# Performance work log

Measured on AMD Instinct MI355X. Metric: run time of the kernel, lower is better.

## Reference

```python
import jax, jax.numpy as jnp
import numpy as np

B, N, M, U, L = 2048, 256, 128, 512, 2   # batch, memory locations, memory width, num_units, num_layers
RH, WH, SH = 2, 2, 1                      # read heads, write heads, conv_shift_range
CLIP = 20.0
HEAD_R = M + 3 + (2 * SH + 1)             # 134 = k(M)+beta+g+s(2r+1)+gamma
HEAD_W = HEAD_R + 2 * M                   # 390 = + erase(M) + add(M)


def setup_inputs():
    key = jax.random.key(0)
    ks = jax.random.split(key, 12)
    def nrm(k, shape, s=0.05):
        return jax.random.normal(k, shape, jnp.float32) * s
    return {
        "X": jax.random.normal(ks[0], (B, U), jnp.float32),
        "m0": nrm(ks[1], (1, N, M), 0.5),
        "H0": nrm(ks[2], (L, 1, U)),
        "C0": nrm(ks[3], (L, 1, U)),
        "R0": nrm(ks[4], (RH, 1, M)),
        "A0": nrm(ks[5], (RH + WH, 1, N)),
        "W_prep": nrm(ks[6], (M * RH, U)),
        "b_prep": jnp.zeros((U,), jnp.float32),
        "W_lstm": nrm(ks[7], (L, 3 * U, 4 * U)),
        "b_lstm": jnp.zeros((L, 4 * U), jnp.float32),
        "W_r": nrm(ks[8], (U, RH * HEAD_R)),
        "b_r": jnp.zeros((RH * HEAD_R,), jnp.float32),
        "W_w": nrm(ks[9], (U, WH * HEAD_W)),
        "b_w": jnp.zeros((WH * HEAD_W,), jnp.float32),
        "W_ou": nrm(ks[10], (U + RH * M, U)),
        "b_ou": jnp.zeros((U,), jnp.float32),
    }


def _addressing(k, beta, g, s, gamma, m, a_prev):
    # k [B,M], beta/g/gamma [B], s [B,2*SH+1], m [B,N,M], a_prev [B,N]
    inner = jnp.einsum('bnm,bm->bn', m, k)
    k_norm = jnp.sqrt(jnp.sum(k * k, axis=1, keepdims=True))   # [B,1]
    m_norm = jnp.sqrt(jnp.sum(m * m, axis=2))                  # [B,N]
    K = inner / (k_norm * m_norm + 1e-8)
    w_c = jax.nn.softmax(beta[:, None] * K, axis=1)            # exp/sum in source == softmax
    w_g = g[:, None] * w_c + (1.0 - g[:, None]) * a_prev
    # The stacked-slice s_matrix in the source is exactly circular convolution:
    # w_conv[i] = sum_d s_d * w_g[(i - d) mod N], d in {0..SH, -SH..-1} matching s layout.
    shifts = list(range(0, SH + 1)) + list(range(-SH, 0))
    w_conv = sum(s[:, j:j + 1] * jnp.roll(w_g, shifts[j], axis=1) for j in range(2 * SH + 1))
    w_sharp = w_conv ** gamma[:, None]
    return w_sharp / jnp.sum(w_sharp, axis=1, keepdims=True)


def reference(X, m0, H0, C0, R0, A0, W_prep, b_prep, W_lstm, b_lstm,
              W_r, b_r, W_w, b_w, W_ou, b_ou):
    b = X.shape[0]
    m = jnp.broadcast_to(m0, (b, N, M))
    R_prev = [jnp.broadcast_to(jnp.tanh(R0[i]), (b, M)) for i in range(RH)]
    A_prev = [jnp.broadcast_to(jax.nn.softmax(A0[i], axis=-1), (b, N)) for i in range(RH + WH)]

    # controller
    h = jnp.concatenate(R_prev, axis=1) @ W_prep + b_prep
    for l in range(L):
        x_in = jnp.concatenate([X, h], axis=1)                              # [B,2U]
        h_prev = jnp.broadcast_to(H0[l], (b, U))
        c_prev = jnp.broadcast_to(C0[l], (b, U))
        z = jnp.concatenate([x_in, h_prev], axis=1) @ W_lstm[l] + b_lstm[l]  # [B,4U]
        i_g, f_g, g_g, o_g = jnp.split(z, 4, axis=1)
        c = jax.nn.sigmoid(f_g) * c_prev + jax.nn.sigmoid(i_g) * jnp.tanh(g_g)
        h = jax.nn.sigmoid(o_g) * jnp.tanh(c)
    h = jnp.clip(h, -CLIP, CLIP)

    r_heads = (h @ W_r + b_r).reshape(b, RH, HEAD_R)
    w_heads = (h @ W_w + b_w).reshape(b, WH, HEAD_W)
    heads = [r_heads[:, i] for i in range(RH)] + [w_heads[:, i] for i in range(WH)]

    A_t = []
    for ii, hd in enumerate(heads):
        A_t.append(_addressing(
            k=jnp.tanh(hd[:, :M]),
            beta=jax.nn.softplus(hd[:, M]),
            g=jax.nn.sigmoid(hd[:, M + 1]),
            s=jax.nn.softmax(hd[:, M + 2:M + 2 + 2 * SH + 1], axis=-1),
            gamma=jax.nn.softplus(hd[:, M + 2 + 2 * SH + 1]),
            m=m, a_prev=A_prev[ii]))

    # reads from old memory
    R_t = [jnp.einsum('bn,bnm->bm', A_t[i], m) for i in range(RH)]

    # sequential erase/add writes
    m_t = m
    for ii in range(WH):
        w = A_t[RH + ii][:, :, None]                                  # [B,N,1]
        del_v = jax.nn.sigmoid(w_heads[:, ii, -2 * M:-M])[:, None, :]  # [B,1,M]
        add_v = jnp.tanh(w_heads[:, ii, -M:])[:, None, :]
        m_t = m_t * (1.0 - w * del_v) + w * add_v

    y = jnp.clip(jnp.concatenate([h] + R_t, axis=1) @ W_ou + b_ou, -CLIP, CLIP)
    return y, m_t
```

## Files before the change

kernel.cpp:

```cpp
#include <hip/hip_runtime.h>
#include <math.h>

static constexpr int Bn = 2048;
static constexpr int Nn = 256;
static constexpr int Mn = 128;
static constexpr int Un = 512;

static constexpr size_t OFF_MNORM = 4608;
static constexpr size_t OFF_APREV = 4864;
static constexpr size_t OFF_BIASH = 5888;
static constexpr size_t OFF_KMAT  = 16384;
static constexpr size_t OFF_HEADS = OFF_KMAT + 2097152;
static constexpr size_t OFF_AT    = OFF_HEADS + 2146304;
static constexpr size_t OFF_ERA   = OFF_AT + 1048576;
static constexpr size_t OFF_ADD   = OFF_ERA + 524288;
static constexpr size_t OFF_XHB   = OFF_ADD + 524288;
static constexpr size_t OFF_HCAT  = OFF_XHB + 1048576;
static constexpr size_t OFF_W0T   = OFF_HCAT + 1048576;
static constexpr size_t OFF_W1T   = OFF_W0T + 524288;
static constexpr size_t OFF_WRWT  = OFF_W1T + 1048576;
static constexpr size_t OFF_WCOMB = OFF_WRWT + 294912;
static constexpr size_t OFF_WR2T  = OFF_WCOMB + 262144;
static constexpr size_t OFF_M0B   = OFF_WR2T + 65536;
static constexpr size_t OFF_ZPART = OFF_M0B + 16384;
static constexpr size_t OFF_YH    = OFF_ZPART + 32768;

static constexpr int P_X0  = 0;
static constexpr int P_M0  = 512;
static constexpr int P_W0  = 528;
static constexpr int P_W1  = 1552;
static constexpr int P_WR2 = 3600;
static constexpr int P_CA  = 3728;
static constexpr int P_ZC  = 3729;
static constexpr int P_END = 3793;

static constexpr int M_L0  = 0;
static constexpr int M_ZX  = 512;
static constexpr int M_PF  = 1024;
static constexpr int M_WRr = 1056;
static constexpr int M_WRw = 1200;
static constexpr int M_WOU = 1600;
static constexpr int M_ZC1 = 1856;
static constexpr int M_END = 1920;

static constexpr int H_HD  = 0;
static constexpr int H_YH  = 288;
static constexpr int H_END = 416;

static constexpr int T_OUT = 0;
static constexpr int T_MEM = 128;
static constexpr int T_END = 384;

#define DEV __device__ __forceinline__

typedef __attribute__((ext_vector_type(8))) short bf16x8;
typedef __attribute__((ext_vector_type(4))) float f32x4;
typedef __attribute__((ext_vector_type(8))) unsigned short ushort8;
typedef unsigned int u32;

DEV float sigf(float x) { return 1.0f / (1.0f + expf(-x)); }
DEV float softplusf(float x) { return x > 20.0f ? x : log1pf(expf(x)); }
DEV unsigned short f2bf(float f) {
    unsigned u = __float_as_uint(f);
    u = (u + 0x7FFFu + ((u >> 16) & 1u)) >> 16;
    return (unsigned short)u;
}
DEV float b2f(unsigned short u) { return __uint_as_float((u32)u << 16); }
DEV void gload16(const unsigned short* g, unsigned short* l) {
    __builtin_amdgcn_global_load_lds(
        (const __attribute__((address_space(1))) u32*)g,
        (__attribute__((address_space(3))) u32*)l, 16, 0, 0);
}

DEV float blk_reduce_max(float v, float* red) {
    int tid = threadIdx.x;
    red[tid] = v; __syncthreads();
    for (int s = (int)blockDim.x >> 1; s > 0; s >>= 1) {
        if (tid < s) red[tid] = fmaxf(red[tid], red[tid + s]);
        __syncthreads();
    }
    float r = red[0]; __syncthreads();
    return r;
}
DEV float blk_reduce_sum(float v, float* red) {
    int tid = threadIdx.x;
    red[tid] = v; __syncthreads();
    for (int s = (int)blockDim.x >> 1; s > 0; s >>= 1) {
        if (tid < s) red[tid] += red[tid + s];
        __syncthreads();
    }
    float r = red[0]; __syncthreads();
    return r;
}

DEV float wv_sum(float v) {
    #pragma unroll
    for (int off = 32; off; off >>= 1) v += __shfl_xor(v, off);
    return v;
}
DEV float wv_max(float v) {
    #pragma unroll
    for (int off = 32; off; off >>= 1) v = fmaxf(v, __shfl_xor(v, off));
    return v;
}
DEV float blk_sum4(float v, float* red4) {
    v = wv_sum(v);
    int w = threadIdx.x >> 6;
    if ((threadIdx.x & 63) == 0) red4[w] = v;
    __syncthreads();
    float r = red4[0] + red4[1] + red4[2] + red4[3];
    __syncthreads();
    return r;
}
DEV float blk_max4(float v, float* red4) {
    v = wv_max(v);
    int w = threadIdx.x >> 6;
    if ((threadIdx.x & 63) == 0) red4[w] = v;
    __syncthreads();
    float r = fmaxf(fmaxf(red4[0], red4[1]), fmaxf(red4[2], red4[3]));
    __syncthreads();
    return r;
}

#define GEMM_SHARED                                                             \
    __shared__ __align__(16) unsigned short As[2][64 * 64];                     \
    __shared__ __align__(16) unsigned short Ws[2][128 * 64];

#define GEMM_REGS                                                               \
    const int tid  = threadIdx.x;                                               \
    const int lane = tid & 63;                                                  \
    const int wave = tid >> 6;                                                  \
    const int wr = wave >> 1, wc = wave & 1;                                    \
    const int ke = ((tid & 7) * 8) ^ (((tid >> 3) & 7) << 3);                   \
    const int frow = lane & 15;                                                 \
    const int fko  = (lane >> 4) * 8;                                           \
    const int fxm  = (frow & 7) << 3;                                           \
    f32x4 acc[2][4];                                                            \
    _Pragma("unroll")                                                           \
    for (int i = 0; i < 2; ++i)                                                 \
        _Pragma("unroll")                                                       \
        for (int j = 0; j < 4; ++j) acc[i][j] = (f32x4){0.f, 0.f, 0.f, 0.f};

#define GEMM_STAGE(buf, k0)                                                     \
    {                                                                           \
        _Pragma("unroll")                                                       \
        for (int q = 0; q < 2; ++q)                                             \
            gload16(A  + (size_t)(row0 + q * 32 + (tid >> 3)) * lda + (k0) + ke,\
                    &As[buf][q * 2048 + tid * 8]);                              \
        _Pragma("unroll")                                                       \
        for (int q = 0; q < 4; ++q)                                             \
            gload16(Wt + (size_t)(col0 + q * 32 + (tid >> 3)) * ldw + (k0) + ke,\
                    &Ws[buf][q * 2048 + tid * 8]);                              \
    }

#define GEMM_FRAGS_AND_MFMA(Ab, Wb)                                             \
    {                                                                           \
        bf16x8 af[2][2], wf[2][4];                                              \
        _Pragma("unroll")                                                       \
        for (int kk = 0; kk < 2; ++kk) {                                        \
            _Pragma("unroll")                                                   \
            for (int i = 0; i < 2; ++i) {                                       \
                int fr = wr * 32 + i * 16 + frow;                               \
                af[kk][i] = *(const bf16x8*)&(Ab)[fr * 64 + ((kk * 32 + fko) ^ fxm)]; \
            }                                                                   \
            _Pragma("unroll")                                                   \
            for (int j = 0; j < 4; ++j) {                                       \
                int fr = wc * 64 + j * 16 + frow;                               \
                wf[kk][j] = *(const bf16x8*)&(Wb)[fr * 64 + ((kk * 32 + fko) ^ fxm)]; \
            }                                                                   \
        }                                                                       \
        __builtin_amdgcn_s_setprio(1);                                          \
        _Pragma("unroll")                                                       \
        for (int kk = 0; kk < 2; ++kk)                                          \
            _Pragma("unroll")                                                   \
            for (int i = 0; i < 2; ++i)                                         \
                _Pragma("unroll")                                               \
                for (int j = 0; j < 4; ++j)                                     \
                    acc[i][j] = __builtin_amdgcn_mfma_f32_16x16x32_bf16(        \
                        af[kk][i], wf[kk][j], acc[i][j], 0, 0, 0);              \
        __builtin_amdgcn_s_setprio(0);                                          \
    }

#define GEMM_MAINLOOP(Kr)                                                       \
    {                                                                           \
        const int nt = (Kr) >> 6;                                               \
        int cur = 0;                                                            \
        GEMM_STAGE(0, 0);                                                       \
        for (int t = 0; t < nt; ++t) {                                          \
            if (t + 1 < nt) {                                                   \
                GEMM_STAGE(cur ^ 1, (t + 1) * 64);                              \
                asm volatile("s_waitcnt vmcnt(6)" ::: "memory");                \
            } else {                                                            \
                asm volatile("s_waitcnt vmcnt(0)" ::: "memory");                \
            }                                                                   \
            __builtin_amdgcn_sched_barrier(0);                                  \
            __builtin_amdgcn_s_barrier();                                       \
            __builtin_amdgcn_sched_barrier(0);                                  \
            GEMM_FRAGS_AND_MFMA(As[cur], Ws[cur]);                              \
            __builtin_amdgcn_sched_barrier(0);                                  \
            __builtin_amdgcn_s_barrier();                                       \
            cur ^= 1;                                                           \
        }                                                                       \
    }

#define LSTM_EPILOGUE(zc, doclip, houtp, ldhv, ZXP)                             \
    {                                                                           \
        const int uu = lane & 15;                                               \
        const int q  = (col0 >> 6) + wc;                                        \
        const int uq = q * 16 + uu;                                             \
        const float c0v = c0[(zc) * 512 + uq];                                  \
        float bg[4];                                                            \
        _Pragma("unroll")                                                       \
        for (int g = 0; g < 4; ++g) {                                           \
            int j = g * 512 + q * 16 + uu;                                      \
            float a = b_lstm[(zc) * 2048 + j];                                  \
            _Pragma("unroll")                                                   \
            for (int p = 0; p < 8; ++p)                                         \
                a += zpart[((size_t)(zc) * 8 + p) * 2048 + j];                  \
            bg[g] = a;                                                          \
        }                                                                       \
        _Pragma("unroll")                                                       \
        for (int i = 0; i < 2; ++i) {                                           \
            int rbase = row0 + wr * 32 + i * 16 + (lane >> 4) * 4;              \
            _Pragma("unroll")                                                   \
            for (int r = 0; r < 4; ++r) {                                       \
                float z0 = 0.f, z1 = 0.f, z2 = 0.f, z3 = 0.f;                   \
                if (ZXP) {                                                      \
                    const unsigned short* zr = (ZXP) +                          \
                        (size_t)(rbase + r) * 2048 + q * 64 + uu;               \
                    z0 = b2f(zr[0]);  z1 = b2f(zr[16]);                         \
                    z2 = b2f(zr[32]); z3 = b2f(zr[48]);                         \
                }                                                               \
                float ig = acc[i][0][r] + bg[0] + z0;                           \
                float fg = acc[i][1][r] + bg[1] + z1;                           \
                float gg = acc[i][2][r] + bg[2] + z2;                           \
                float og = acc[i][3][r] + bg[3] + z3;                           \
                float c = sigf(fg) * c0v + sigf(ig) * tanhf(gg);                \
                float h = sigf(og) * tanhf(c);                                  \
                if (doclip) h = fminf(fmaxf(h, -20.f), 20.f);                   \
                (houtp)[(size_t)(rbase + r) * (ldhv) + uq] = f2bf(h);           \
            }                                                                   \
        }                                                                       \
    }

DEV void dev_cvt8(const float* src, int lds, unsigned short* dst, int ldd,
                  int c8, int bloc, int tid)
{
    size_t idx = (size_t)bloc * 256 + tid;
    size_t r = idx / c8, c = (idx % c8) * 8;
    const float* s = src + r * lds + c;
    float4 v0 = *(const float4*)s;
    float4 v1 = *(const float4*)(s + 4);
    ushort8 o;
    o[0] = f2bf(v0.x); o[1] = f2bf(v0.y); o[2] = f2bf(v0.z); o[3] = f2bf(v0.w);
    o[4] = f2bf(v1.x); o[5] = f2bf(v1.y); o[6] = f2bf(v1.z); o[7] = f2bf(v1.w);
    *(ushort8*)(dst + r * ldd + c) = o;
}

DEV void dev_cvtT(const float* src, int R, int C, int lds,
                  unsigned short* dst, int ldd, int mode, int bx, int by,
                  int tid, float* t )
{
    const int x = tid & 31;
    for (int y = tid >> 5; y < 32; y += 8) {
        int r = by * 32 + y, c = bx * 32 + x;
        int scol = c;
        if (mode) scol = ((c >> 4) & 3) * 512 + (c >> 6) * 16 + (c & 15);
        t[y * 33 + x] = (r < R && c < C) ? src[(size_t)r * lds + scol] : 0.f;
    }
    __syncthreads();
    for (int y = tid >> 5; y < 32; y += 8) {
        int c = bx * 32 + y, r = by * 32 + x;
        if (c < C && r < R) dst[(size_t)c * ldd + r] = f2bf(t[x * 33 + y]);
    }
}

__global__ __launch_bounds__(256) void k_prep(
    const float* __restrict__ X, const float* __restrict__ m0,
    const float* __restrict__ H0, const float* __restrict__ R0,
    const float* __restrict__ A0, const float* __restrict__ W_prep,
    const float* __restrict__ b_prep, const float* __restrict__ W_lstm,
    const float* __restrict__ b_r, const float* __restrict__ b_w,
    const float* __restrict__ W_ou, float* __restrict__ ws)
{
    __shared__ float sh[32 * 33 + 64];
    const int bid = blockIdx.x, tid = threadIdx.x;
    unsigned short* XHB  = (unsigned short*)(ws + OFF_XHB);
    unsigned short* W0T  = (unsigned short*)(ws + OFF_W0T);
    unsigned short* W1T  = (unsigned short*)(ws + OFF_W1T);
    unsigned short* WR2T = (unsigned short*)(ws + OFF_WR2T);
    unsigned short* M0B  = (unsigned short*)(ws + OFF_M0B);

    if (bid < P_M0) {
        dev_cvt8(X, 512, XHB, 1024, 64, bid - P_X0, tid);
    } else if (bid < P_W0) {
        dev_cvt8(m0, 128, M0B, 128, 16, bid - P_M0, tid);
    } else if (bid < P_W1) {
        int s = bid - P_W0;
        dev_cvtT(W_lstm, 512, 2048, 2048, W0T, 512, 1, s & 63, s >> 6, tid, sh);
    } else if (bid < P_WR2) {
        int s = bid - P_W1;
        dev_cvtT(W_lstm + (size_t)1536 * 2048, 1024, 2048, 2048, W1T, 1024, 1,
                 s & 63, s >> 6, tid, sh);
    } else if (bid < P_CA) {
        int s = bid - P_WR2;
        dev_cvtT(W_ou + (size_t)512 * 512, 256, 512, 512, WR2T, 256, 0,
                 s & 15, s >> 4, tid, sh);
    } else if (bid < P_ZC) {
        float* red = sh;
        for (int i = 0; i < 4; ++i) {
            float v = A0[i * 256 + tid];
            float mx = blk_reduce_max(v, red);
            float e = expf(v - mx);
            float s = blk_reduce_sum(e, red);
            ws[OFF_APREV + i * 256 + tid] = e / s;
        }
        float acc = 0.f;
        for (int m = 0; m < 128; ++m) {
            float t = m0[(size_t)tid * 128 + m];
            acc = fmaf(t, t, acc);
        }
        ws[OFF_MNORM + tid] = sqrtf(acc);
        for (int j = tid; j < 1152; j += 256)
            ws[OFF_BIASH + j] = (j < 268) ? b_r[j] : (j < 1048 ? b_w[j - 268] : 0.f);
    } else {
        int sub = bid - P_ZC;
        int colb = sub & 7, up = sub >> 3;
        int j = colb * 256 + tid;
        float acc = 0.f;
        if (up < 4) {
            sh[256 + tid] = tanhf(R0[tid]);
            __syncthreads();
            if (tid < 128) {
                int u = up * 128 + tid;
                float a = b_prep[u];
                for (int k = 0; k < 256; ++k)
                    a = fmaf(sh[256 + k], W_prep[(size_t)k * 512 + u], a);
                sh[tid] = a;
            }
            __syncthreads();
            const int u0 = up * 128;
            #pragma unroll 4
            for (int t = 0; t < 128; ++t)
                acc = fmaf(sh[t], W_lstm[(size_t)(512 + u0 + t) * 2048 + j], acc);
        } else {
            const int u0 = up * 128;
            #pragma unroll 4
            for (int t = 0; t < 128; ++t)
                acc = fmaf(H0[u0 - 512 + t],
                           W_lstm[(size_t)(512 + u0 + t) * 2048 + j], acc);
        }
        (ws + OFF_ZPART)[(size_t)up * 2048 + j] = acc;
    }
}

__global__ __launch_bounds__(256) void k_mid(
    const float* __restrict__ W_lstm, const float* __restrict__ W_r,
    const float* __restrict__ W_w, const float* __restrict__ W_ou,
    const float* __restrict__ H0, const float* __restrict__ b_lstm,
    const float* __restrict__ c0, float* __restrict__ ws)
{
    GEMM_SHARED
    const int s = blockIdx.x;
    float* sh = (float*)&As[0][0];
    unsigned short* XHB   = (unsigned short*)(ws + OFF_XHB);
    unsigned short* W0T   = (unsigned short*)(ws + OFF_W0T);
    unsigned short* W1T   = (unsigned short*)(ws + OFF_W1T);
    unsigned short* WRWT  = (unsigned short*)(ws + OFF_WRWT);
    unsigned short* WCOMB = (unsigned short*)(ws + OFF_WCOMB);
    unsigned short* WR2T  = (unsigned short*)(ws + OFF_WR2T);
    unsigned short* M0B   = (unsigned short*)(ws + OFF_M0B);
    unsigned short* ZX    = (unsigned short*)(ws + OFF_KMAT);
    const float* zpart    = ws + OFF_ZPART;

    if (s < M_WRr) {
        const unsigned short *A, *Wt;
        int lda, ldw, row0, col0, Kr, mode;
        unsigned short* pCb = nullptr;
        if (s < M_ZX) {
            mode = 0;
            A = XHB;  lda = 1024; Wt = W0T; ldw = 512;
            row0 = (s & 31) * 64; col0 = (s >> 5) * 128; Kr = 512;
        } else if (s < M_PF) {
            int p = s - M_ZX;
            mode = 1;
            A = XHB;  lda = 1024; Wt = W1T; ldw = 1024;
            row0 = (p & 31) * 64; col0 = (p >> 5) * 128; Kr = 512;
        } else {
            int p = s - M_PF;
            mode = 2;
            int pz = p >> 4, py = (p >> 3) & 1, px = p & 7;
            A = WR2T + pz * 128; lda = 256; Wt = M0B; ldw = 128;
            row0 = px * 64; col0 = py * 128; Kr = 128;
            pCb = WCOMB + 512 + pz * 256;
        }
        GEMM_REGS
        GEMM_MAINLOOP(Kr)
        if (mode == 0) {
            unsigned short* hout = XHB + 512;
            const unsigned short* zxn = nullptr;
            LSTM_EPILOGUE(0, 0, hout, 1024, zxn)
        } else if (mode == 1) {
            #pragma unroll
            for (int i = 0; i < 2; ++i) {
                int m0r = row0 + wr * 32 + i * 16 + (lane >> 4) * 4;
                #pragma unroll
                for (int j = 0; j < 4; ++j) {
                    int n = col0 + wc * 64 + j * 16 + (lane & 15);
                    #pragma unroll
                    for (int r = 0; r < 4; ++r)
                        ZX[(size_t)(m0r + r) * 2048 + n] = f2bf(acc[i][j][r]);
                }
            }
        } else {
            #pragma unroll
            for (int i = 0; i < 2; ++i) {
                int m0r = row0 + wr * 32 + i * 16 + (lane >> 4) * 4;
                #pragma unroll
                for (int j = 0; j < 4; ++j) {
                    int n = col0 + wc * 64 + j * 16 + (lane & 15);
                    #pragma unroll
                    for (int r = 0; r < 4; ++r)
                        pCb[(size_t)(m0r + r) * 1024 + n] = f2bf(acc[i][j][r]);
                }
            }
        }
    } else if (s < M_WRw) {
        int s2 = s - M_WRr;
        dev_cvtT(W_r, 512, 268, 268, WRWT, 512, 0, s2 % 9, s2 / 9, threadIdx.x, sh);
    } else if (s < M_WOU) {
        int s3 = s - M_WRw;
        dev_cvtT(W_w, 512, 780, 780, WRWT + (size_t)268 * 512, 512, 0,
                 s3 % 25, s3 / 25, threadIdx.x, sh);
    } else if (s < M_ZC1) {
        int s4 = s - M_WOU;
        dev_cvtT(W_ou, 512, 512, 512, WCOMB, 1024, 0, s4 & 15, s4 >> 4,
                 threadIdx.x, sh);
    } else {
        int s5 = s - M_ZC1;
        int colb = s5 & 7, up = s5 >> 3;
        int j = colb * 256 + threadIdx.x;
        const int u0 = up * 64;
        const float* W1 = W_lstm + (size_t)1536 * 2048;
        float acc = 0.f;
        #pragma unroll 4
        for (int t = 0; t < 64; ++t)
            acc = fmaf(H0[512 + u0 + t], W1[(size_t)(1024 + u0 + t) * 2048 + j], acc);
        (ws + OFF_ZPART)[((size_t)8 + up) * 2048 + j] = acc;
    }
}

__global__ __launch_bounds__(256) void gemm_lstm(
    const unsigned short* __restrict__ A, int lda,
    const unsigned short* __restrict__ Wt, int ldw,
    const float* __restrict__ zpart, const float* __restrict__ b_lstm,
    const float* __restrict__ c0, const unsigned short* __restrict__ ZXP,
    unsigned short* __restrict__ hout)
{
    GEMM_SHARED
    const int row0 = blockIdx.x * 64;
    const int col0 = blockIdx.y * 128;
    GEMM_REGS
    GEMM_MAINLOOP(512)
    LSTM_EPILOGUE(1, 1, hout, 1024, ZXP)
}

__global__ __launch_bounds__(256) void k_heads(
    const unsigned short* __restrict__ HCAT,
    const unsigned short* __restrict__ WRWT,
    const unsigned short* __restrict__ WCOMB,
    const float* __restrict__ biash,
    float* __restrict__ heads, float* __restrict__ yh)
{
    GEMM_SHARED
    const int s = blockIdx.x;
    const unsigned short* A = HCAT;  const int lda = 1024;
    const unsigned short* Wt;
    int ldw, row0, col0;
    if (s < H_YH) {
        Wt = WRWT; ldw = 512;
        row0 = (s & 31) * 64; col0 = (s >> 5) * 128;
    } else {
        int p = s - H_YH;
        Wt = WCOMB; ldw = 1024;
        row0 = (p & 31) * 64; col0 = (p >> 5) * 128;
    }
    GEMM_REGS
    GEMM_MAINLOOP(512)
    if (s < H_YH) {
        #pragma unroll
        for (int i = 0; i < 2; ++i) {
            int m0r = row0 + wr * 32 + i * 16 + (lane >> 4) * 4;
            #pragma unroll
            for (int j = 0; j < 4; ++j) {
                int n = col0 + wc * 64 + j * 16 + (lane & 15);
                if (n >= 1048) continue;
                float bv = biash[n];
                #pragma unroll
                for (int r = 0; r < 4; ++r)
                    heads[(size_t)(m0r + r) * 1048 + n] = acc[i][j][r] + bv;
            }
        }
    } else {
        #pragma unroll
        for (int i = 0; i < 2; ++i) {
            int m0r = row0 + wr * 32 + i * 16 + (lane >> 4) * 4;
            #pragma unroll
            for (int j = 0; j < 4; ++j) {
                int n = col0 + wc * 64 + j * 16 + (lane & 15);
                #pragma unroll
                for (int r = 0; r < 4; ++r)
                    yh[(size_t)(m0r + r) * 512 + n] = acc[i][j][r];
            }
        }
    }
}

__global__ __launch_bounds__(256) void gemm_kmat(
    const float* __restrict__ heads,
    const unsigned short* __restrict__ M0B,
    float* __restrict__ C)
{
    GEMM_SHARED
    const int row0 = blockIdx.x * 64;
    const int col0 = blockIdx.y * 128;
    GEMM_REGS

#define KMAT_STAGE(buf, k0)                                                     \
    {                                                                           \
        _Pragma("unroll")                                                       \
        for (int q = 0; q < 2; ++q) {                                           \
            int R = row0 + q * 32 + (tid >> 3);                                 \
            int b = R >> 2, ih = R & 3;                                         \
            int cb = (ih < 2) ? ih * 134 : 268 + (ih - 2) * 390;                \
            const float* hp = heads + (size_t)b * 1048 + cb + (k0) + ke;        \
            ushort8 o;                                                          \
            _Pragma("unroll")                                                   \
            for (int j = 0; j < 8; ++j) o[j] = f2bf(tanhf(hp[j]));              \
            *(ushort8*)&As[buf][q * 2048 + tid * 8] = o;                        \
        }                                                                       \
        _Pragma("unroll")                                                       \
        for (int q = 0; q < 4; ++q)                                             \
            gload16(M0B + (size_t)(col0 + q * 32 + (tid >> 3)) * 128 + (k0) + ke,\
                    &Ws[buf][q * 2048 + tid * 8]);                              \
    }

    int cur = 0;
    KMAT_STAGE(0, 0);
    for (int t = 0; t < 2; ++t) {
        __syncthreads();
        if (t == 0) KMAT_STAGE(1, 64);
        GEMM_FRAGS_AND_MFMA(As[cur], Ws[cur]);
        cur ^= 1;
    }
#undef KMAT_STAGE
    #pragma unroll
    for (int i = 0; i < 2; ++i) {
        int m0r = row0 + wr * 32 + i * 16 + (lane >> 4) * 4;
        #pragma unroll
        for (int j = 0; j < 4; ++j) {
            int n = col0 + wc * 64 + j * 16 + (lane & 15);
            #pragma unroll
            for (int r = 0; r < 4; ++r)
                C[(size_t)(m0r + r) * 256 + n] = acc[i][j][r];
        }
    }
}

__global__ __launch_bounds__(256) void k_addr(
    const float* __restrict__ heads, const float* __restrict__ kmat,
    const float* __restrict__ mnorm, const float* __restrict__ aprev,
    float* __restrict__ at, unsigned short* __restrict__ hcat,
    float* __restrict__ era, float* __restrict__ addv)
{
    __shared__ float red4[4];
    __shared__ float wgs[256];
    __shared__ float sc[6];
    const int b = blockIdx.x, i = blockIdx.y, tid = threadIdx.x;
    const int cb = (i < 2) ? i * 134 : 268 + (i - 2) * 390;
    const float* hd = heads + (size_t)b * 1048 + cb;
    float kv = (tid < 128) ? tanhf(hd[tid]) : 0.f;
    float kn = sqrtf(blk_sum4(kv * kv, red4));
    if (i >= 2 && tid < 128) {
        era [((size_t)b * 2 + (i - 2)) * 128 + tid] = sigf(hd[134 + tid]);
        addv[((size_t)b * 2 + (i - 2)) * 128 + tid] = tanhf(hd[262 + tid]);
    }
    if (tid == 0) {
        sc[0] = softplusf(hd[128]);
        sc[1] = sigf(hd[129]);
        float v0 = hd[130], v1 = hd[131], v2 = hd[132];
        float mx = fmaxf(v0, fmaxf(v1, v2));
        float e0 = expf(v0 - mx), e1 = expf(v1 - mx), e2 = expf(v2 - mx);
        float ssum = e0 + e1 + e2;
        sc[2] = e0 / ssum; sc[3] = e1 / ssum; sc[4] = e2 / ssum;
        sc[5] = softplusf(hd[133]);
    }
    __syncthreads();
    const float beta = sc[0], g = sc[1], s0 = sc[2], s1 = sc[3], s2 = sc[4],
                gamma = sc[5];
    float inner = kmat[((size_t)b * 4 + i) * 256 + tid];
    float K = inner / (kn * mnorm[tid] + 1e-8f);
    float x = beta * K;
    float mx = blk_max4(x, red4);
    float e = expf(x - mx);
    float se = blk_sum4(e, red4);
    float wc = e / se;
    float wg = g * wc + (1.f - g) * aprev[i * 256 + tid];
    wgs[tid] = wg;
    __syncthreads();
    float wconv = s0 * wg + s1 * wgs[(tid + 255) & 255] + s2 * wgs[(tid + 1) & 255];
    float wsh = powf(wconv, gamma);
    float ssum = blk_sum4(wsh, red4);
    float w = wsh / ssum;
    if (i < 2) hcat[(size_t)b * 1024 + 512 + i * 256 + tid] = f2bf(w);
    else       at[((size_t)(i - 2) * Bn + b) * 256 + tid] = w;
}

__global__ __launch_bounds__(256) void k_tail(
    const unsigned short* __restrict__ HCAT,
    const unsigned short* __restrict__ WCOMB,
    const float* __restrict__ yh, const float* __restrict__ b_ou,
    const float* __restrict__ m0, const float* __restrict__ at,
    const float* __restrict__ era, const float* __restrict__ addv,
    float* __restrict__ out)
{
    GEMM_SHARED
    const int s = blockIdx.x;
    if (s < T_MEM) {
        const unsigned short* A  = HCAT + 512;        const int lda = 1024;
        const unsigned short* Wt = WCOMB + 512;       const int ldw = 1024;
        const int row0 = (s & 31) * 64;
        const int col0 = (s >> 5) * 128;
        GEMM_REGS
        GEMM_MAINLOOP(512)
        #pragma unroll
        for (int i = 0; i < 2; ++i) {
            int m0r = row0 + wr * 32 + i * 16 + (lane >> 4) * 4;
            #pragma unroll
            for (int j = 0; j < 4; ++j) {
                int n = col0 + wc * 64 + j * 16 + (lane & 15);
                if (n >= 512) continue;
                float bv = b_ou[n];
                #pragma unroll
                for (int r = 0; r < 4; ++r) {
                    float v = acc[i][j][r] + bv + yh[(size_t)(m0r + r) * 512 + n];
                    out[(size_t)(m0r + r) * 512 + n] = fminf(fmaxf(v, -20.f), 20.f);
                }
            }
        }
    } else {
        const int tid = threadIdx.x;
        const int b0 = (s - T_MEM) * 8;
        float (*at_s)[8][256] = (float(*)[8][256])(&As[0][0]);
        float (*er_s)[8][128] = (float(*)[8][128])(&Ws[0][0]);
        float (*ad_s)[8][128] = (float(*)[8][128])(&Ws[0][4096]);
        for (int t = tid; t < 1024; t += 256) {
            int i = t >> 9, rem = t & 511;
            int bb = rem >> 6, n4 = rem & 63;
            ((float4*)&at_s[i][bb][0])[n4] =
                ((const float4*)(at + ((size_t)i * Bn + b0 + bb) * 256))[n4];
        }
        for (int t = tid; t < 512; t += 256) {
            int i = t >> 8, rem = t & 255;
            int bb = rem >> 5, m4 = rem & 31;
            ((float4*)&er_s[i][bb][0])[m4] =
                ((const float4*)(era + ((size_t)(b0 + bb) * 2 + i) * 128))[m4];
            ((float4*)&ad_s[i][bb][0])[m4] =
                ((const float4*)(addv + ((size_t)(b0 + bb) * 2 + i) * 128))[m4];
        }
        __syncthreads();
        const float4* m0v = (const float4*)m0;
        float4* outv = (float4*)(out + (size_t)Bn * Un);
        for (int pos = tid; pos < 8192; pos += 256) {
            int mq = pos & 31, n = pos >> 5;
            float4 t0 = m0v[pos];
            #pragma unroll
            for (int bb = 0; bb < 8; ++bb) {
                float w0 = at_s[0][bb][n], w1 = at_s[1][bb][n];
                float4 e0 = *(const float4*)&er_s[0][bb][mq * 4];
                float4 a0 = *(const float4*)&ad_s[0][bb][mq * 4];
                float4 e1 = *(const float4*)&er_s[1][bb][mq * 4];
                float4 a1 = *(const float4*)&ad_s[1][bb][mq * 4];
                float4 t = t0;
#define UPD(c) { t.c = t.c * (1.f - w0 * e0.c) + w0 * a0.c; \
                 t.c = t.c * (1.f - w1 * e1.c) + w1 * a1.c; }
                UPD(x) UPD(y) UPD(z) UPD(w)
#undef UPD
                __builtin_nontemporal_store(*(f32x4*)&t,
                    (f32x4*)&outv[(size_t)(b0 + bb) * 8192 + pos]);
            }
        }
    }
}

extern "C" void kernel_launch(void* const* d_in, const int* in_sizes, int n_in,
                              void* d_out, int out_size, void* d_ws, size_t ws_size,
                              hipStream_t stream)
{
    const float* X      = (const float*)d_in[0];
    const float* m0     = (const float*)d_in[1];
    const float* H0     = (const float*)d_in[2];
    const float* C0     = (const float*)d_in[3];
    const float* R0     = (const float*)d_in[4];
    const float* A0     = (const float*)d_in[5];
    const float* W_prep = (const float*)d_in[6];
    const float* b_prep = (const float*)d_in[7];
    const float* W_lstm = (const float*)d_in[8];
    const float* b_lstm = (const float*)d_in[9];
    const float* W_r    = (const float*)d_in[10];
    const float* b_r    = (const float*)d_in[11];
    const float* W_w    = (const float*)d_in[12];
    const float* b_w    = (const float*)d_in[13];
    const float* W_ou   = (const float*)d_in[14];
    const float* b_ou   = (const float*)d_in[15];
    float* ws  = (float*)d_ws;
    float* out = (float*)d_out;

    unsigned short* XHB   = (unsigned short*)(ws + OFF_XHB);
    unsigned short* HCAT  = (unsigned short*)(ws + OFF_HCAT);
    unsigned short* W1T   = (unsigned short*)(ws + OFF_W1T);
    unsigned short* WRWT  = (unsigned short*)(ws + OFF_WRWT);
    unsigned short* WCOMB = (unsigned short*)(ws + OFF_WCOMB);
    unsigned short* M0B   = (unsigned short*)(ws + OFF_M0B);
    unsigned short* ZX    = (unsigned short*)(ws + OFF_KMAT);

    k_prep<<<P_END, 256, 0, stream>>>(
        X, m0, H0, R0, A0, W_prep, b_prep, W_lstm, b_r, b_w, W_ou, ws);

    k_mid<<<M_END, 256, 0, stream>>>(
        W_lstm, W_r, W_w, W_ou, H0, b_lstm, C0, ws);

    gemm_lstm<<<dim3(32, 16), 256, 0, stream>>>(
        XHB + 512, 1024, W1T + 512, 1024, ws + OFF_ZPART, b_lstm, C0, ZX, HCAT);

    k_heads<<<H_END, 256, 0, stream>>>(
        HCAT, WRWT, WCOMB, ws + OFF_BIASH, ws + OFF_HEADS, ws + OFF_YH);

    gemm_kmat<<<dim3(128, 2), 256, 0, stream>>>(
        ws + OFF_HEADS, M0B, ws + OFF_KMAT);

    k_addr<<<dim3(Bn, 4), 256, 0, stream>>>(
        ws + OFF_HEADS, ws + OFF_KMAT, ws + OFF_MNORM, ws + OFF_APREV,
        ws + OFF_AT, HCAT, ws + OFF_ERA, ws + OFF_ADD);

    k_tail<<<T_END, 256, 0, stream>>>(
        HCAT, WCOMB, ws + OFF_YH, b_ou, m0, ws + OFF_AT, ws + OFF_ERA,
        ws + OFF_ADD, out);
}
```

Measured before the change: 173.5 us.

## Fuse key-vs-memory GEMM into heads kernel by recomputing key projections in-block

```diff
diff --git a/kernel.cpp b/kernel.cpp
--- a/kernel.cpp
+++ b/kernel.cpp
@@ -45,7 +45,8 @@
 
 static constexpr int H_HD  = 0;
 static constexpr int H_YH  = 288;
-static constexpr int H_END = 416;
+static constexpr int H_KM  = 416;
+static constexpr int H_END = 672;
 
 static constexpr int T_OUT = 0;
 static constexpr int T_MEM = 128;
@@ -465,104 +466,113 @@
     LSTM_EPILOGUE(1, 1, hout, 1024, ZXP)
 }
 
-__global__ __launch_bounds__(256) void k_heads(
+__global__ __launch_bounds__(256) void k_hk(
     const unsigned short* __restrict__ HCAT,
     const unsigned short* __restrict__ WRWT,
     const unsigned short* __restrict__ WCOMB,
+    const unsigned short* __restrict__ M0B,
     const float* __restrict__ biash,
-    float* __restrict__ heads, float* __restrict__ yh)
+    float* __restrict__ heads, float* __restrict__ yh,
+    float* __restrict__ kmat)
 {
     GEMM_SHARED
     const int s = blockIdx.x;
-    const unsigned short* A = HCAT;  const int lda = 1024;
-    const unsigned short* Wt;
-    int ldw, row0, col0;
-    if (s < H_YH) {
-        Wt = WRWT; ldw = 512;
-        row0 = (s & 31) * 64; col0 = (s >> 5) * 128;
+    if (s < H_KM) {
+        const unsigned short* A = HCAT;  const int lda = 1024;
+        const unsigned short* Wt;
+        int ldw, row0, col0;
+        if (s < H_YH) {
+            Wt = WRWT; ldw = 512;
+            row0 = (s & 31) * 64; col0 = (s >> 5) * 128;
+        } else {
+            int p = s - H_YH;
+            Wt = WCOMB; ldw = 1024;
+            row0 = (p & 31) * 64; col0 = (p >> 5) * 128;
+        }
+        GEMM_REGS
+        GEMM_MAINLOOP(512)
+        if (s < H_YH) {
+            #pragma unroll
+            for (int i = 0; i < 2; ++i) {
+                int m0r = row0 + wr * 32 + i * 16 + (lane >> 4) * 4;
+                #pragma unroll
+                for (int j = 0; j < 4; ++j) {
+                    int n = col0 + wc * 64 + j * 16 + (lane & 15);
+                    if (n >= 1048) continue;
+                    float bv = biash[n];
+                    #pragma unroll
+                    for (int r = 0; r < 4; ++r)
+                        heads[(size_t)(m0r + r) * 1048 + n] = acc[i][j][r] + bv;
+                }
+            }
+        } else {
+            #pragma unroll
+            for (int i = 0; i < 2; ++i) {
+                int m0r = row0 + wr * 32 + i * 16 + (lane >> 4) * 4;
+                #pragma unroll
+                for (int j = 0; j < 4; ++j) {
+                    int n = col0 + wc * 64 + j * 16 + (lane & 15);
+                    #pragma unroll
+                    for (int r = 0; r < 4; ++r)
+                        yh[(size_t)(m0r + r) * 512 + n] = acc[i][j][r];
+                }
+            }
+        }
     } else {
-        int p = s - H_YH;
-        Wt = WCOMB; ldw = 1024;
-        row0 = (p & 31) * 64; col0 = (p >> 5) * 128;
-    }
-    GEMM_REGS
-    GEMM_MAINLOOP(512)
-    if (s < H_YH) {
+        int p = s - H_KM;
+        const int ih = p >> 6;
+        const int bt = (p >> 1) & 31;
+        const int nt = p & 1;
+        const int cb = (ih < 2) ? ih * 134 : 268 + (ih - 2) * 390;
+        const unsigned short* A  = HCAT;          const int lda = 1024;
+        const unsigned short* Wt = WRWT + (size_t)cb * 512;  const int ldw = 512;
+        const int row0 = bt * 64;
+        const int col0 = 0;
+        GEMM_REGS
+        GEMM_MAINLOOP(512)
+
         #pragma unroll
         for (int i = 0; i < 2; ++i) {
-            int m0r = row0 + wr * 32 + i * 16 + (lane >> 4) * 4;
+            int rloc = wr * 32 + i * 16 + (lane >> 4) * 4;
             #pragma unroll
             for (int j = 0; j < 4; ++j) {
-                int n = col0 + wc * 64 + j * 16 + (lane & 15);
-                if (n >= 1048) continue;
-                float bv = biash[n];
+                int kloc = wc * 64 + j * 16 + (lane & 15);
+                float bk = biash[cb + kloc];
+                int buf = kloc >> 6;
+                int lg = (kloc >> 3) & 7, off = kloc & 7;
+                #pragma unroll
+                for (int r = 0; r < 4; ++r) {
+                    int row = rloc + r;
+                    As[buf][row * 64 + (((lg ^ (row & 7)) << 3) | off)] =
+                        f2bf(tanhf(acc[i][j][r] + bk));
+                }
+            }
+        }
+        #pragma unroll
+        for (int i = 0; i < 2; ++i)
+            #pragma unroll
+            for (int j = 0; j < 4; ++j) acc[i][j] = (f32x4){0.f, 0.f, 0.f, 0.f};
+        const int nb0 = nt * 128;
+        #pragma unroll
+        for (int kt = 0; kt < 2; ++kt)
+            #pragma unroll
+            for (int q = 0; q < 4; ++q)
+                gload16(M0B + (size_t)(nb0 + q * 32 + (tid >> 3)) * 128 + kt * 64 + ke,
+                        &Ws[kt][q * 2048 + tid * 8]);
+        __syncthreads();
+        GEMM_FRAGS_AND_MFMA(As[0], Ws[0]);
+        GEMM_FRAGS_AND_MFMA(As[1], Ws[1]);
+        #pragma unroll
+        for (int i = 0; i < 2; ++i) {
+            int rloc = wr * 32 + i * 16 + (lane >> 4) * 4;
+            #pragma unroll
+            for (int j = 0; j < 4; ++j) {
+                int n = nb0 + wc * 64 + j * 16 + (lane & 15);
                 #pragma unroll
                 for (int r = 0; r < 4; ++r)
-                    heads[(size_t)(m0r + r) * 1048 + n] = acc[i][j][r] + bv;
-            }
-        }
-    } else {
-        #pragma unroll
-        for (int i = 0; i < 2; ++i) {
-            int m0r = row0 + wr * 32 + i * 16 + (lane >> 4) * 4;
-            #pragma unroll
-            for (int j = 0; j < 4; ++j) {
-                int n = col0 + wc * 64 + j * 16 + (lane & 15);
-                #pragma unroll
-                for (int r = 0; r < 4; ++r)
-                    yh[(size_t)(m0r + r) * 512 + n] = acc[i][j][r];
-            }
-        }
-    }
-}
-
-__global__ __launch_bounds__(256) void gemm_kmat(
-    const float* __restrict__ heads,
-    const unsigned short* __restrict__ M0B,
-    float* __restrict__ C)
-{
-    GEMM_SHARED
-    const int row0 = blockIdx.x * 64;
-    const int col0 = blockIdx.y * 128;
-    GEMM_REGS
-
-#define KMAT_STAGE(buf, k0)                                                     \
-    {                                                                           \
-        _Pragma("unroll")                                                       \
-        for (int q = 0; q < 2; ++q) {                                           \
-            int R = row0 + q * 32 + (tid >> 3);                                 \
-            int b = R >> 2, ih = R & 3;                                         \
-            int cb = (ih < 2) ? ih * 134 : 268 + (ih - 2) * 390;                \
-            const float* hp = heads + (size_t)b * 1048 + cb + (k0) + ke;        \
-            ushort8 o;                                                          \
-            _Pragma("unroll")                                                   \
-            for (int j = 0; j < 8; ++j) o[j] = f2bf(tanhf(hp[j]));              \
-            *(ushort8*)&As[buf][q * 2048 + tid * 8] = o;                        \
-        }                                                                       \
-        _Pragma("unroll")                                                       \
-        for (int q = 0; q < 4; ++q)                                             \
-            gload16(M0B + (size_t)(col0 + q * 32 + (tid >> 3)) * 128 + (k0) + ke,\
-                    &Ws[buf][q * 2048 + tid * 8]);                              \
-    }
-
-    int cur = 0;
-    KMAT_STAGE(0, 0);
-    for (int t = 0; t < 2; ++t) {
-        __syncthreads();
-        if (t == 0) KMAT_STAGE(1, 64);
-        GEMM_FRAGS_AND_MFMA(As[cur], Ws[cur]);
-        cur ^= 1;
-    }
-#undef KMAT_STAGE
-    #pragma unroll
-    for (int i = 0; i < 2; ++i) {
-        int m0r = row0 + wr * 32 + i * 16 + (lane >> 4) * 4;
-        #pragma unroll
-        for (int j = 0; j < 4; ++j) {
-            int n = col0 + wc * 64 + j * 16 + (lane & 15);
-            #pragma unroll
-            for (int r = 0; r < 4; ++r)
-                C[(size_t)(m0r + r) * 256 + n] = acc[i][j][r];
+                    kmat[((size_t)ih * 2048 + row0 + rloc + r) * 256 + n] =
+                        acc[i][j][r];
+            }
         }
     }
 }
@@ -598,7 +608,7 @@
     __syncthreads();
     const float beta = sc[0], g = sc[1], s0 = sc[2], s1 = sc[3], s2 = sc[4],
                 gamma = sc[5];
-    float inner = kmat[((size_t)b * 4 + i) * 256 + tid];
+    float inner = kmat[((size_t)i * 2048 + b) * 256 + tid];
     float K = inner / (kn * mnorm[tid] + 1e-8f);
     float x = beta * K;
     float mx = blk_max4(x, red4);
@@ -733,11 +743,9 @@
     gemm_lstm<<<dim3(32, 16), 256, 0, stream>>>(
         XHB + 512, 1024, W1T + 512, 1024, ws + OFF_ZPART, b_lstm, C0, ZX, HCAT);
 
-    k_heads<<<H_END, 256, 0, stream>>>(
-        HCAT, WRWT, WCOMB, ws + OFF_BIASH, ws + OFF_HEADS, ws + OFF_YH);
-
-    gemm_kmat<<<dim3(128, 2), 256, 0, stream>>>(
-        ws + OFF_HEADS, M0B, ws + OFF_KMAT);
+    k_hk<<<H_END, 256, 0, stream>>>(
+        HCAT, WRWT, WCOMB, M0B, ws + OFF_BIASH, ws + OFF_HEADS, ws + OFF_YH,
+        ws + OFF_KMAT);
 
     k_addr<<<dim3(Bn, 4), 256, 0, stream>>>(
         ws + OFF_HEADS, ws + OFF_KMAT, ws + OFF_MNORM, ws + OFF_APREV,
```

Result: faster. 167.1 us, median of 2 (-3.6%).
